# Kernel optimization log

Hardware: AMD Instinct MI355X
Metric: run time of the kernel (lower is better)

The kernel has to match this reference:

```python
import jax, jax.numpy as jnp
import numpy as np
import math

B, S, H, NH = 4, 1024, 1024, 16
DH = H // NH
G = 100  # native graph size


def setup_inputs() -> dict:
    key = jax.random.key(0)
    ks = jax.random.split(key, 12)
    sc = 1.0 / math.sqrt(H)
    return {
        "v": jax.random.normal(ks[0], (B, S, H), jnp.float32),
        "k": jax.random.normal(ks[1], (B, S, H), jnp.float32),
        "q": jax.random.normal(ks[2], (B, S, H), jnp.float32),
        "mask": jax.random.randint(ks[3], (B, 1, 1, S), 0, 2) == 1,
        "graph": jax.random.uniform(ks[4], (B, G, G), jnp.float32),
        "Wq": jax.random.normal(ks[5], (H, H), jnp.float32) * sc,
        "bq": jnp.zeros((H,), jnp.float32),
        "Wk": jax.random.normal(ks[6], (H, H), jnp.float32) * sc,
        "bk": jnp.zeros((H,), jnp.float32),
        "Wv": jax.random.normal(ks[7], (H, H), jnp.float32) * sc,
        "bv": jnp.zeros((H,), jnp.float32),
        "Wm": jax.random.normal(ks[8], (H, H), jnp.float32) * sc,
        "bm": jnp.zeros((H,), jnp.float32),
    }


def _heads(x, W, b):
    # [B,S,H] -> [B,NH,S,DH]
    y = x @ W + b
    return y.reshape(B, S, NH, DH).transpose(0, 2, 1, 3)


def reference(v, k, q, mask, graph, Wq, bq, Wk, bk, Wv, bv, Wm, bm):
    qh = _heads(q, Wq, bq)
    kh = _heads(k, Wk, bk)
    vh = _heads(v, Wv, bv)
    scores = jnp.einsum("bhqd,bhkd->bhqk", qh, kh) / math.sqrt(DH)
    # pad 100x100 graph to SxS (zeros outside top-left block), as in torch source
    if S > G:
        graph = jnp.zeros((B, S, S), graph.dtype).at[:, :G, :G].set(graph)
    # scores - scores*graph, then mask fill and softmax
    scores = scores - scores * graph[:, None, :, :]
    scores = jnp.where(mask, jnp.float32(-1e9), scores)
    att = jax.nn.softmax(scores, axis=-1)  # dropout is identity in eval
    out = jnp.einsum("bhqk,bhkd->bhqd", att, vh)
    out = out.transpose(0, 2, 1, 3).reshape(B, S, H)
    return out @ Wm + bm
```

## Files before the change

### kernel.cpp

```cpp
#include <hip/hip_runtime.h>
#include <hip/hip_bf16.h>
#include <cstdio>

#define S_ 1024
#define H_ 1024
#define NH_ 16
#define DH_ 64
#define G_ 100

typedef __attribute__((ext_vector_type(8))) short bf16x8;
typedef __attribute__((ext_vector_type(4))) short bf16x4;
typedef __attribute__((ext_vector_type(4))) float f32x4;

__device__ __forceinline__ f32x4 mfma16(bf16x8 a, bf16x8 b, f32x4 c) {
  return __builtin_amdgcn_mfma_f32_16x16x32_bf16(a, b, c, 0, 0, 0);
}

__device__ __forceinline__ short f2bf(float f) {
  union { float f; unsigned int i; } x;
  x.f = f;
  unsigned int r = x.i + 0x7fff + ((x.i >> 16) & 1);
  return (short)(r >> 16);
}

__device__ __forceinline__ unsigned cvtpk(float lo, float hi) {
  unsigned r;
  asm("v_cvt_pk_bf16_f32 %0, %1, %2" : "=v"(r) : "v"(lo), "v"(hi));
  return r;
}

__device__ __forceinline__ float exp2hw(float x) {
  float r;
  asm("v_exp_f32 %0, %1" : "=v"(r) : "v"(x));
  return r;
}

__device__ __forceinline__ void gload16(const void* g, void* l) {
  __builtin_amdgcn_global_load_lds(
      (const __attribute__((address_space(1))) unsigned int*)g,
      (__attribute__((address_space(3))) unsigned int*)l, 16, 0, 0);
}

__global__ __launch_bounds__(256) void compact(
    const int* __restrict__ mask, int* __restrict__ idx,
    int* __restrict__ cnts) {
  __shared__ int ps[256];
  __shared__ int scnt;
  const int b = blockIdx.x, t = threadIdx.x;
  int4 mv = reinterpret_cast<const int4*>(mask + b * S_)[t];
  const int k0 = (mv.x == 0), k1 = (mv.y == 0), k2 = (mv.z == 0),
            k3 = (mv.w == 0);
  const int c = k0 + k1 + k2 + k3;
  ps[t] = c;
  __syncthreads();
  for (int off = 1; off < 256; off <<= 1) {
    int v = (t >= off) ? ps[t - off] : 0;
    __syncthreads();
    ps[t] += v;
    __syncthreads();
  }
  int j = ps[t] - c;
  const int s0 = t * 4;
  if (k0) idx[b * S_ + j++] = s0;
  if (k1) idx[b * S_ + j++] = s0 + 1;
  if (k2) idx[b * S_ + j++] = s0 + 2;
  if (k3) idx[b * S_ + j++] = s0 + 3;
  if (t == 255) {
    scnt = ps[255];
    cnts[b] = ps[255];
  }
  __syncthreads();
  for (int j2 = scnt + t; j2 < S_; j2 += 256) idx[b * S_ + j2] = 0;
  int c100 = (k0 && s0 < G_) + (k1 && s0 + 1 < G_) + (k2 && s0 + 2 < G_) +
             (k3 && s0 + 3 < G_);
  ps[t] = c100;
  __syncthreads();
  for (int off = 128; off > 0; off >>= 1) {
    if (t < off) ps[t] += ps[t + off];
    __syncthreads();
  }
  if (t == 0) cnts[4 + b] = ps[0];
}

__global__ __launch_bounds__(256) void transpose_w(
    const float* __restrict__ W0, const float* __restrict__ W1,
    const float* __restrict__ W2, const float* __restrict__ W3,
    short* __restrict__ T0, short* __restrict__ T1,
    short* __restrict__ T2, short* __restrict__ T3) {
  __shared__ short tile[64][72];
  const float* W = (blockIdx.z == 0) ? W0 : (blockIdx.z == 1) ? W1
                 : (blockIdx.z == 2) ? W2 : W3;
  short* T = (blockIdx.z == 0) ? T0 : (blockIdx.z == 1) ? T1
           : (blockIdx.z == 2) ? T2 : T3;
  const int t = threadIdx.x;
  const int r0 = t >> 3;
  const int c8 = (t & 7) * 8;
  const int kbase = blockIdx.x * 64, nbase = blockIdx.y * 64;
#pragma unroll
  for (int p = 0; p < 2; ++p) {
    int r = p * 32 + r0;
    const float* src = W + (size_t)(kbase + r) * H_ + nbase + c8;
    f32x4 u0 = *reinterpret_cast<const f32x4*>(src);
    f32x4 u1 = *reinterpret_cast<const f32x4*>(src + 4);
#pragma unroll
    for (int j = 0; j < 4; ++j) {
      tile[r][c8 + j] = f2bf(u0[j]);
      tile[r][c8 + 4 + j] = f2bf(u1[j]);
    }
  }
  __syncthreads();
#pragma unroll
  for (int p = 0; p < 2; ++p) {
    int r = p * 32 + r0;
    bf16x8 o;
#pragma unroll
    for (int j = 0; j < 8; ++j) o[j] = tile[c8 + j][r];
    *reinterpret_cast<bf16x8*>(T + (size_t)(nbase + r) * H_ + kbase + c8) = o;
  }
}

__global__ __launch_bounds__(256, 3) void qkv128f(
    const float* __restrict__ A0, const float* __restrict__ A1,
    const float* __restrict__ A2, const short* __restrict__ W0,
    const short* __restrict__ W1, const short* __restrict__ W2,
    const float* __restrict__ b0, const float* __restrict__ b1,
    const float* __restrict__ b2, short* __restrict__ O0,
    short* __restrict__ O1, short* __restrict__ O2,
    const int* __restrict__ idx, const int* __restrict__ cnts) {
  __shared__ float Af[2][128 * 32];
  __shared__ short Bs[2][128 * 32];
  const int z = blockIdx.z;
  const float* A  = (z == 0) ? A0 : (z == 1) ? A1 : A2;
  const short* Bt = (z == 0) ? W0 : (z == 1) ? W1 : W2;
  const float* bias = (z == 0) ? b0 : (z == 1) ? b1 : b2;
  short* Cb = (z == 0) ? O0 : (z == 1) ? O1 : O2;
  const float scale = (z == 0) ? 0.18033688f : 1.0f;
  const int K = H_;
  const int t = threadIdx.x;
  const int l = t & 63, w = t >> 6;
  const int lr = l & 15, lg = l >> 4;
  const int lx = lr & 7;
  const int lk = (lr >> 1) & 3;
  const int wm = w >> 1, wn = w & 1;
  const int bm = blockIdx.x * 128, bn = blockIdx.y * 128;
  const int bidx = bm >> 10;
  const int jrow = bm & 1023;
  const int cnt = (z == 0) ? 1024 : cnts[bidx];
  f32x4 acc[4][4];
#pragma unroll
  for (int i = 0; i < 4; ++i)
#pragma unroll
    for (int j = 0; j < 4; ++j) acc[i][j] = (f32x4){0.f, 0.f, 0.f, 0.f};

  if (jrow < cnt) {
    const int ar = t >> 3;
    const int acol = ((t & 7) ^ (ar & 7)) * 4;
    const int* idxb = idx + bidx * 1024;
    const float* Abp[4];
#pragma unroll
    for (int p = 0; p < 4; ++p) {
      const int j = jrow + ar + p * 32;
      const int srow = (z == 0) ? j : idxb[j];
      Abp[p] = A + ((size_t)(bidx << 10) + srow) * K + acol;
    }
    const int br = t >> 2;
    const short* Bb =
        Bt + (size_t)(bn + br) * K + ((t & 3) ^ ((br >> 1) & 3)) * 8;

    auto stage = [&](int buf, int kb) {
#pragma unroll
      for (int p = 0; p < 4; ++p)
        gload16(Abp[p] + kb, (char*)&Af[buf][0] + p * 4096 + t * 16);
#pragma unroll
      for (int p = 0; p < 2; ++p)
        gload16(Bb + (size_t)p * 64 * K + kb,
                (char*)&Bs[buf][0] + p * 4096 + t * 16);
    };

    stage(0, 0);
    __syncthreads();
    const int NT = K >> 5;
    for (int tt = 0; tt < NT; ++tt) {
      const int cur = tt & 1;
      bf16x8 af[4], bfr[4];
#pragma unroll
      for (int mi = 0; mi < 4; ++mi) {
        const int row = wm * 64 + mi * 16 + lr;
        const float* Ar = &Af[cur][row * 32];
        f32x4 alo =
            *reinterpret_cast<const f32x4*>(Ar + (((lg * 2) ^ lx) * 4));
        f32x4 ahi =
            *reinterpret_cast<const f32x4*>(Ar + (((lg * 2 + 1) ^ lx) * 4));
        union { unsigned u[4]; bf16x8 v; } c;
        c.u[0] = cvtpk(alo[0], alo[1]);
        c.u[1] = cvtpk(alo[2], alo[3]);
        c.u[2] = cvtpk(ahi[0], ahi[1]);
        c.u[3] = cvtpk(ahi[2], ahi[3]);
        af[mi] = c.v;
      }
#pragma unroll
      for (int ni = 0; ni < 4; ++ni) {
        const int rb = wn * 64 + ni * 16 + lr;
        bfr[ni] = *reinterpret_cast<const bf16x8*>(
            &Bs[cur][rb * 32 + ((lg ^ lk) * 8)]);
      }
      if (tt + 1 < NT) stage(cur ^ 1, (tt + 1) << 5);
#pragma unroll
      for (int mi = 0; mi < 4; ++mi)
#pragma unroll
        for (int ni = 0; ni < 4; ++ni)
          acc[mi][ni] = mfma16(af[mi], bfr[ni], acc[mi][ni]);
      __syncthreads();
    }
  }
#pragma unroll
  for (int mi = 0; mi < 4; ++mi)
#pragma unroll
    for (int ni = 0; ni < 4; ++ni) {
      int col = bn + wn * 64 + ni * 16 + lr;
      float bv = bias[col];
      int h = col >> 6, d = col & 63;
      if (z == 2) {
        int row0 = bm + wm * 64 + mi * 16 + lg * 4;
        int b = row0 >> 10, s0 = row0 & 1023;
        bf16x4 pk;
#pragma unroll
        for (int r = 0; r < 4; ++r) pk[r] = f2bf(acc[mi][ni][r] + bv);
        *reinterpret_cast<bf16x4*>(
            Cb + (((size_t)(b * NH_ + h)) * DH_ + d) * S_ + s0) = pk;
      } else {
#pragma unroll
        for (int r = 0; r < 4; ++r) {
          int row = bm + wm * 64 + mi * 16 + lg * 4 + r;
          int b = row >> 10, s = row & 1023;
          Cb[(((size_t)(b * NH_ + h)) * S_ + s) * DH_ + d] =
              f2bf((acc[mi][ni][r] + bv) * scale);
        }
      }
    }
}

__global__ __launch_bounds__(256) void out64(
    const short* __restrict__ A, const short* __restrict__ Bt,
    const float* __restrict__ bias, float* __restrict__ Cf) {
  __shared__ short As[2][64 * 32];
  __shared__ short Bs[2][128 * 32];
  const int K = H_, N = H_;
  const int t = threadIdx.x;
  const int l = t & 63, w = t >> 6;
  const int lr = l & 15, lg = l >> 4;
  const int lk = (lr >> 1) & 3;
  const int wm = w >> 1, wn = w & 1;
  const int bm = blockIdx.x * 64, bn = blockIdx.y * 128;
  f32x4 acc[2][4];
#pragma unroll
  for (int i = 0; i < 2; ++i)
#pragma unroll
    for (int j = 0; j < 4; ++j) acc[i][j] = (f32x4){0.f, 0.f, 0.f, 0.f};
  const int sr = t >> 2;
  const int ss = ((t & 3) ^ ((sr >> 1) & 3)) * 8;
  const short* Ab = A + (size_t)(bm + sr) * K + ss;
  const short* Bb = Bt + (size_t)(bn + sr) * K + ss;

  auto stage = [&](int buf, int kb) {
    gload16(Ab + kb, (char*)&As[buf][0] + t * 16);
    gload16(Bb + kb, (char*)&Bs[buf][0] + t * 16);
    gload16(Bb + (size_t)64 * K + kb, (char*)&Bs[buf][0] + 4096 + t * 16);
  };

  stage(0, 0);
  __syncthreads();
  const int NT = K >> 5;
  for (int tt = 0; tt < NT; ++tt) {
    const int cur = tt & 1;
    bf16x8 af[2], bfr[4];
#pragma unroll
    for (int mi = 0; mi < 2; ++mi) {
      const int row = wm * 32 + mi * 16 + lr;
      af[mi] = *reinterpret_cast<const bf16x8*>(
          &As[cur][row * 32 + ((lg ^ lk) * 8)]);
    }
#pragma unroll
    for (int ni = 0; ni < 4; ++ni) {
      const int rb = wn * 64 + ni * 16 + lr;
      bfr[ni] = *reinterpret_cast<const bf16x8*>(
          &Bs[cur][rb * 32 + ((lg ^ lk) * 8)]);
    }
    if (tt + 1 < NT) stage(cur ^ 1, (tt + 1) << 5);
#pragma unroll
    for (int mi = 0; mi < 2; ++mi)
#pragma unroll
      for (int ni = 0; ni < 4; ++ni)
        acc[mi][ni] = mfma16(af[mi], bfr[ni], acc[mi][ni]);
    __syncthreads();
  }
#pragma unroll
  for (int mi = 0; mi < 2; ++mi)
#pragma unroll
    for (int ni = 0; ni < 4; ++ni) {
      int col = bn + wn * 64 + ni * 16 + lr;
      float bv = bias[col];
#pragma unroll
      for (int r = 0; r < 4; ++r) {
        int row = bm + wm * 32 + mi * 16 + lg * 4 + r;
        Cf[(size_t)row * N + col] = acc[mi][ni][r] + bv;
      }
    }
}

__global__ __launch_bounds__(256) void attn(
    const short* __restrict__ Qh, const short* __restrict__ Kh,
    const short* __restrict__ VhT, const float* __restrict__ graph,
    const int* __restrict__ idx, const int* __restrict__ cnts,
    short* __restrict__ ctx) {
  __shared__ short Kb[64 * 64];
  __shared__ short Vb[64 * 64];
  __shared__ short P[4 * 16 * 64];
  __shared__ float maskf[S_];
  const int lin = blockIdx.x;
  const int gid = (lin & 7) * 128 + (lin >> 3);
  const int bh = gid >> 4, qt = gid & 15;
  const int b = bh >> 4, h = bh & 15;
  const int t = threadIdx.x, w = t >> 6, l = t & 63;
  const int lr = l & 15, lg = l >> 4;
  const int lx = lr & 7;
  const int q0 = qt * 64 + w * 16;
  const int qg = q0 + lr;
  short* Pw = P + w * 1024;
  const int cnt = cnts[b];
  const int cnt100 = cnts[4 + b];
  const int kend = ((cnt + 63) >> 6) << 6;
  const int* idxb = idx + b * 1024;
  const short* Qrow = Qh + ((size_t)bh * S_ + qg) * DH_;
  bf16x8 qf0 = *reinterpret_cast<const bf16x8*>(Qrow + lg * 8);
  bf16x8 qf1 = *reinterpret_cast<const bf16x8*>(Qrow + 32 + lg * 8);
  f32x4 o[4];
#pragma unroll
  for (int i = 0; i < 4; ++i) o[i] = (f32x4){0.f, 0.f, 0.f, 0.f};
  float llp = 0.f;

  const int rs = t >> 2;
  const int ga = (t & 3) + ((rs & 1) << 2);
  const int gb = ga ^ 4;
  const int sw0 = ((ga ^ (rs & 7)) * 8);
  const int sw1 = ((gb ^ (rs & 7)) * 8);
  const short* Ksrc0 = Kh + ((size_t)bh * S_ + rs) * DH_ + ga * 8;
  const short* Ksrc1 = Kh + ((size_t)bh * S_ + rs) * DH_ + gb * 8;
  const short* Vsrc0 = VhT + ((size_t)bh * DH_ + rs) * S_ + ga * 8;
  const short* Vsrc1 = VhT + ((size_t)bh * DH_ + rs) * S_ + gb * 8;

  {
    const int s0 = t * 4;
    f32x4 mo;
    mo.x = (s0 < cnt) ? -16.f : -1.0e9f;
    mo.y = (s0 + 1 < cnt) ? -16.f : -1.0e9f;
    mo.z = (s0 + 2 < cnt) ? -16.f : -1.0e9f;
    mo.w = (s0 + 3 < cnt) ? -16.f : -1.0e9f;
    reinterpret_cast<f32x4*>(maskf)[t] = mo;
  }
  {
    int4 ka = *reinterpret_cast<const int4*>(Ksrc0);
    int4 kb2 = *reinterpret_cast<const int4*>(Ksrc1);
    int4 va = *reinterpret_cast<const int4*>(Vsrc0);
    int4 vb2 = *reinterpret_cast<const int4*>(Vsrc1);
    *reinterpret_cast<int4*>(&Kb[rs * 64 + sw0]) = ka;
    *reinterpret_cast<int4*>(&Kb[rs * 64 + sw1]) = kb2;
    *reinterpret_cast<int4*>(&Vb[rs * 64 + sw0]) = va;
    *reinterpret_cast<int4*>(&Vb[rs * 64 + sw1]) = vb2;
  }
  __syncthreads();

  for (int kc = 0; kc < kend; kc += 64) {
    const bool pf = (kc + 64 < kend);
    int4 ka, kb2, va, vb2;
    if (pf) {
      ka = *reinterpret_cast<const int4*>(Ksrc0 + (size_t)(kc + 64) * DH_);
      kb2 = *reinterpret_cast<const int4*>(Ksrc1 + (size_t)(kc + 64) * DH_);
      va = *reinterpret_cast<const int4*>(Vsrc0 + kc + 64);
      vb2 = *reinterpret_cast<const int4*>(Vsrc1 + kc + 64);
    }
    f32x4 sacc[4];
    __builtin_amdgcn_s_setprio(1);
#pragma unroll
    for (int mf = 0; mf < 4; ++mf) {
      const int rk = mf * 16 + lr;
      bf16x8 k0 = *reinterpret_cast<const bf16x8*>(
          &Kb[rk * 64 + ((lg ^ lx) * 8)]);
      bf16x8 k1 = *reinterpret_cast<const bf16x8*>(
          &Kb[rk * 64 + (((4 + lg) ^ lx) * 8)]);
      f32x4 sa = (f32x4){0.f, 0.f, 0.f, 0.f};
      sa = mfma16(k0, qf0, sa);
      sa = mfma16(k1, qf1, sa);
      sacc[mf] = sa;
    }
    __builtin_amdgcn_s_setprio(0);
    const bool gblk = (q0 < G_) && (kc < cnt100);
    const int pw0 = lr * 64 + (lg & 1) * 4;
#pragma unroll
    for (int mf = 0; mf < 4; ++mf) {
      f32x4 mk = *reinterpret_cast<const f32x4*>(&maskf[kc + mf * 16 + lg * 4]);
      f32x4 sa = sacc[mf];
      if (gblk) {
#pragma unroll
        for (int r = 0; r < 4; ++r) {
          int kgc = kc + mf * 16 + lg * 4 + r;
          if (qg < G_ && kgc < cnt100)
            sa[r] *= (1.f - graph[((size_t)b * G_ + qg) * G_ + idxb[kgc]]);
        }
      }
      float e0 = exp2hw(sa[0] + mk[0]);
      float e1 = exp2hw(sa[1] + mk[1]);
      float e2 = exp2hw(sa[2] + mk[2]);
      float e3 = exp2hw(sa[3] + mk[3]);
      llp += (e0 + e1) + (e2 + e3);
      int2 pk2;
      pk2.x = (int)cvtpk(e0, e1);
      pk2.y = (int)cvtpk(e2, e3);
      *reinterpret_cast<int2*>(
          &Pw[pw0 + (((2 * mf + (lg >> 1)) ^ lx) * 8)]) = pk2;
    }
    __builtin_amdgcn_s_setprio(1);
#pragma unroll
    for (int ks = 0; ks < 2; ++ks) {
      bf16x8 pa = *reinterpret_cast<const bf16x8*>(
          &Pw[lr * 64 + (((ks * 4 + lg) ^ lx) * 8)]);
#pragma unroll
      for (int nf = 0; nf < 4; ++nf) {
        const int rv = nf * 16 + lr;
        bf16x8 vfr = *reinterpret_cast<const bf16x8*>(
            &Vb[rv * 64 + (((ks * 4 + lg) ^ lx) * 8)]);
        o[nf] = mfma16(pa, vfr, o[nf]);
      }
    }
    __builtin_amdgcn_s_setprio(0);
    if (pf) {
      __syncthreads();
      *reinterpret_cast<int4*>(&Kb[rs * 64 + sw0]) = ka;
      *reinterpret_cast<int4*>(&Kb[rs * 64 + sw1]) = kb2;
      *reinterpret_cast<int4*>(&Vb[rs * 64 + sw0]) = va;
      *reinterpret_cast<int4*>(&Vb[rs * 64 + sw1]) = vb2;
      __syncthreads();
    }
  }
  llp += __shfl_xor(llp, 16);
  llp += __shfl_xor(llp, 32);
  float rinv[4];
#pragma unroll
  for (int r = 0; r < 4; ++r)
    rinv[r] = __builtin_amdgcn_rcpf(__shfl(llp, lg * 4 + r, 64));
#pragma unroll
  for (int nf = 0; nf < 4; ++nf)
#pragma unroll
    for (int r = 0; r < 4; ++r) {
      float val = o[nf][r] * rinv[r];
      ctx[((size_t)b * S_ + q0 + lg * 4 + r) * H_ + h * DH_ + nf * 16 + lr] =
          f2bf(val);
    }
}

extern "C" void kernel_launch(void* const* d_in, const int* in_sizes, int n_in,
                              void* d_out, int out_size, void* d_ws, size_t ws_size,
                              hipStream_t stream) {
  const int B = in_sizes[0] / (S_ * H_);
  const int M = B * S_;
  const float* v    = (const float*)d_in[0];
  const float* k    = (const float*)d_in[1];
  const float* q    = (const float*)d_in[2];
  const int*   mask = (const int*)d_in[3];
  const float* graph= (const float*)d_in[4];
  const float* Wq   = (const float*)d_in[5];
  const float* bq   = (const float*)d_in[6];
  const float* Wk   = (const float*)d_in[7];
  const float* bk   = (const float*)d_in[8];
  const float* Wv   = (const float*)d_in[9];
  const float* bv   = (const float*)d_in[10];
  const float* Wm   = (const float*)d_in[11];
  const float* bm   = (const float*)d_in[12];

  short* ws = (short*)d_ws;
  const size_t WSZ = (size_t)H_ * H_;
  const size_t TSZ = (size_t)M * H_;
  short* WqT = ws;
  short* WkT = ws + WSZ;
  short* WvT = ws + 2 * WSZ;
  short* WmT = ws + 3 * WSZ;
  short* Qh  = ws + 4 * WSZ;
  short* Kh  = Qh + TSZ;
  short* VhT = Kh + TSZ;
  short* ctx = VhT + TSZ;
  int*   idxw = (int*)(ctx + TSZ);
  int*   cntw = idxw + 4 * 1024;
  if (ws_size < (4 * WSZ + 4 * TSZ) * sizeof(short) + (4 * 1024 + 8) * 4) {
    fprintf(stderr, "kernel_launch: ws too small (%zu)\n", ws_size);
    return;
  }

  compact<<<dim3(4), 256, 0, stream>>>(mask, idxw, cntw);
  transpose_w<<<dim3(H_ / 64, H_ / 64, 4), 256, 0, stream>>>(
      Wq, Wk, Wv, Wm, WqT, WkT, WvT, WmT);
  qkv128f<<<dim3(M / 128, H_ / 128, 3), 256, 0, stream>>>(
      q, k, v, WqT, WkT, WvT, bq, bk, bv, Qh, Kh, VhT, idxw, cntw);
  attn<<<dim3(1024), 256, 0, stream>>>(Qh, Kh, VhT, graph, idxw, cntw, ctx);
  out64<<<dim3(M / 64, H_ / 128), 256, 0, stream>>>(
      ctx, WmT, bm, (float*)d_out);
}
```

Measured before the change: 101.3 us.

## Load QKV GEMM operands directly from global memory into registers, dropping LDS staging

The QKV projection kernel no longer stages A (fp32 activations) and B (bf16 weights) tiles through double-buffered shared memory with async loads and barriers. Each lane now reads its MFMA fragments straight from global memory each k-step and converts A to bf16 in registers. This removes LDS traffic, swizzling and __syncthreads, and the 3-blocks-per-CU launch bound is dropped. In exchange, each operand row is fetched separately by the waves that need it, so there is no reuse through shared memory and no explicit prefetch to hide global latency.

```diff
diff --git a/kernel.cpp b/kernel.cpp
--- a/kernel.cpp
+++ b/kernel.cpp
@@ -119,7 +119,7 @@
   }
 }
 
-__global__ __launch_bounds__(256, 3) void qkv128f(
+__global__ __launch_bounds__(256) void qkvr(
     const float* __restrict__ A0, const float* __restrict__ A1,
     const float* __restrict__ A2, const short* __restrict__ W0,
     const short* __restrict__ W1, const short* __restrict__ W2,
@@ -127,8 +127,6 @@
     const float* __restrict__ b2, short* __restrict__ O0,
     short* __restrict__ O1, short* __restrict__ O2,
     const int* __restrict__ idx, const int* __restrict__ cnts) {
-  __shared__ float Af[2][128 * 32];
-  __shared__ short Bs[2][128 * 32];
   const int z = blockIdx.z;
   const float* A  = (z == 0) ? A0 : (z == 1) ? A1 : A2;
   const short* Bt = (z == 0) ? W0 : (z == 1) ? W1 : W2;
@@ -139,8 +137,6 @@
   const int t = threadIdx.x;
   const int l = t & 63, w = t >> 6;
   const int lr = l & 15, lg = l >> 4;
-  const int lx = lr & 7;
-  const int lk = (lr >> 1) & 3;
   const int wm = w >> 1, wn = w & 1;
   const int bm = blockIdx.x * 128, bn = blockIdx.y * 128;
   const int bidx = bm >> 10;
@@ -153,44 +149,23 @@
     for (int j = 0; j < 4; ++j) acc[i][j] = (f32x4){0.f, 0.f, 0.f, 0.f};
 
   if (jrow < cnt) {
-    const int ar = t >> 3;
-    const int acol = ((t & 7) ^ (ar & 7)) * 4;
     const int* idxb = idx + bidx * 1024;
-    const float* Abp[4];
-#pragma unroll
-    for (int p = 0; p < 4; ++p) {
-      const int j = jrow + ar + p * 32;
+    const float* Ap[4];
+    const short* Bp[4];
+#pragma unroll
+    for (int i = 0; i < 4; ++i) {
+      const int j = jrow + wm * 64 + i * 16 + lr;
       const int srow = (z == 0) ? j : idxb[j];
-      Abp[p] = A + ((size_t)(bidx << 10) + srow) * K + acol;
-    }
-    const int br = t >> 2;
-    const short* Bb =
-        Bt + (size_t)(bn + br) * K + ((t & 3) ^ ((br >> 1) & 3)) * 8;
-
-    auto stage = [&](int buf, int kb) {
-#pragma unroll
-      for (int p = 0; p < 4; ++p)
-        gload16(Abp[p] + kb, (char*)&Af[buf][0] + p * 4096 + t * 16);
-#pragma unroll
-      for (int p = 0; p < 2; ++p)
-        gload16(Bb + (size_t)p * 64 * K + kb,
-                (char*)&Bs[buf][0] + p * 4096 + t * 16);
-    };
-
-    stage(0, 0);
-    __syncthreads();
-    const int NT = K >> 5;
-    for (int tt = 0; tt < NT; ++tt) {
-      const int cur = tt & 1;
+      Ap[i] = A + ((size_t)(bidx << 10) + srow) * K + lg * 8;
+      Bp[i] = Bt + (size_t)(bn + wn * 64 + i * 16 + lr) * K + lg * 8;
+    }
+#pragma unroll 2
+    for (int kb = 0; kb < K; kb += 32) {
       bf16x8 af[4], bfr[4];
 #pragma unroll
       for (int mi = 0; mi < 4; ++mi) {
-        const int row = wm * 64 + mi * 16 + lr;
-        const float* Ar = &Af[cur][row * 32];
-        f32x4 alo =
-            *reinterpret_cast<const f32x4*>(Ar + (((lg * 2) ^ lx) * 4));
-        f32x4 ahi =
-            *reinterpret_cast<const f32x4*>(Ar + (((lg * 2 + 1) ^ lx) * 4));
+        f32x4 alo = *reinterpret_cast<const f32x4*>(Ap[mi] + kb);
+        f32x4 ahi = *reinterpret_cast<const f32x4*>(Ap[mi] + kb + 4);
         union { unsigned u[4]; bf16x8 v; } c;
         c.u[0] = cvtpk(alo[0], alo[1]);
         c.u[1] = cvtpk(alo[2], alo[3]);
@@ -199,18 +174,13 @@
         af[mi] = c.v;
       }
 #pragma unroll
-      for (int ni = 0; ni < 4; ++ni) {
-        const int rb = wn * 64 + ni * 16 + lr;
-        bfr[ni] = *reinterpret_cast<const bf16x8*>(
-            &Bs[cur][rb * 32 + ((lg ^ lk) * 8)]);
-      }
-      if (tt + 1 < NT) stage(cur ^ 1, (tt + 1) << 5);
+      for (int ni = 0; ni < 4; ++ni)
+        bfr[ni] = *reinterpret_cast<const bf16x8*>(Bp[ni] + kb);
 #pragma unroll
       for (int mi = 0; mi < 4; ++mi)
 #pragma unroll
         for (int ni = 0; ni < 4; ++ni)
           acc[mi][ni] = mfma16(af[mi], bfr[ni], acc[mi][ni]);
-      __syncthreads();
     }
   }
 #pragma unroll
@@ -498,7 +468,7 @@
   compact<<<dim3(4), 256, 0, stream>>>(mask, idxw, cntw);
   transpose_w<<<dim3(H_ / 64, H_ / 64, 4), 256, 0, stream>>>(
       Wq, Wk, Wv, Wm, WqT, WkT, WvT, WmT);
-  qkv128f<<<dim3(M / 128, H_ / 128, 3), 256, 0, stream>>>(
+  qkvr<<<dim3(M / 128, H_ / 128, 3), 256, 0, stream>>>(
       q, k, v, WqT, WkT, WvT, bq, bk, bv, Qh, Kh, VhT, idxw, cntw);
   attn<<<dim3(1024), 256, 0, stream>>>(Qh, Kh, VhT, graph, idxw, cntw, ctx);
   out64<<<dim3(M / 64, H_ / 128), 256, 0, stream>>>(
```

Result: slower. 191.5 us (+88.9%).
